# Optimization experiments

Hardware: AMD Instinct MI355X
Metric: run time of the kernel (lower is better)

The kernel has to match this reference:

```python
import jax, jax.numpy as jnp
import numpy as np

N = 100000      # num nodes
E = 800000      # num edges
IN = 256        # in_features
D = 64          # out_features per head
H = 4           # num_heads
EF = 64         # edge_feats
NET = 8         # num_etype
SLOPE = 0.2     # leaky relu negative slope


def setup_inputs() -> dict:
    key = jax.random.key(0)
    ks = jax.random.split(key, 12)
    s = 0.05
    h = jax.random.normal(ks[0], (N, IN), jnp.float32)
    row = jax.random.randint(ks[1], (E,), 0, N, dtype=jnp.int32)   # src
    col = jax.random.randint(ks[2], (E,), 0, N, dtype=jnp.int32)   # dst
    tp = jax.random.randint(ks[3], (E,), 0, NET, dtype=jnp.int32)  # edge type
    W = jax.random.normal(ks[4], (IN, D * H), jnp.float32) * s
    W_e = jax.random.normal(ks[5], (EF, EF * H), jnp.float32) * s
    edge_emb = jax.random.normal(ks[6], (NET, EF), jnp.float32) * s
    a_l = jax.random.normal(ks[7], (1, H, D), jnp.float32) * s
    a_r = jax.random.normal(ks[8], (1, H, D), jnp.float32) * s
    a_e = jax.random.normal(ks[9], (1, H, EF), jnp.float32) * s
    res_W = jax.random.normal(ks[10], (IN, D * H), jnp.float32) * s
    res_b = jnp.zeros((D * H,), jnp.float32)
    return {"h": h, "W": W, "W_e": W_e, "edge_emb": edge_emb,
            "a_l": a_l, "a_r": a_r, "a_e": a_e,
            "res_W": res_W, "res_b": res_b,
            "row": row, "col": col, "tp": tp}


def reference(h, W, W_e, edge_emb, a_l, a_r, a_e, res_W, res_b, row, col, tp):
    # node projection -> [N, H, D]; nan-guard as in the original
    emb = jnp.nan_to_num((h @ W).reshape(-1, H, D), nan=0.0)
    # edge-type embedding projection -> [NET, H, EF]
    e = (edge_emb @ W_e).reshape(-1, H, EF)
    # per-edge attention logits [E, H]
    h_l = (a_l * emb).sum(-1)[row]
    h_r = (a_r * emb).sum(-1)[col]
    h_e = (a_e * e).sum(-1)[tp]
    att = jax.nn.leaky_relu(h_l + h_r + h_e, SLOPE)
    # segment softmax over edges grouped by destination node
    m = jax.ops.segment_max(att, col, num_segments=N)          # [N, H]
    ex = jnp.exp(att - m[col])                                 # [E, H]
    denom = jax.ops.segment_sum(ex, col, num_segments=N)      # [N, H]
    alpha = ex / denom[col]                                    # [E, H]
    # gather-multiply-scatter message passing: [E, H, D] -> [N, H, D]
    msg = emb[row] * alpha[:, :, None]
    out = jax.ops.segment_sum(msg, col, num_segments=N).reshape(N, H * D)
    # residual linear + elu activation
    out = out + h @ res_W + res_b
    return jax.nn.elu(out)
```

## Files before the change

kernel.cpp:

```cpp
#include <hip/hip_runtime.h>

#define N_NODES 100000
#define E_EDGES 800000
#define IN_F 256
#define D_HEAD 64
#define H_HEADS 4
#define EF_F 64
#define NET_T 8
#define HD 256
#define SLOPE 0.2f
#define NTILES ((N_NODES + 63) / 64)

typedef unsigned short u16;
typedef unsigned long long u64;
typedef __attribute__((ext_vector_type(8))) short bf16x8;
typedef __attribute__((ext_vector_type(4))) float f32x4;

static __device__ __forceinline__ u16 f2bf(float f) {
    unsigned int u = __float_as_uint(f);
    unsigned int r = u + 0x7FFFu + ((u >> 16) & 1u);
    return (u16)(r >> 16);
}
static __device__ __forceinline__ float bf2f(unsigned int u) {
    return __uint_as_float(u << 16);
}

__global__ void k_se(const float* __restrict__ edge_emb, const float* __restrict__ W_e,
                     const float* __restrict__ a_e, float* __restrict__ s_e) {
    int tid = threadIdx.x;
    int t  = tid >> 5;
    int h  = (tid >> 3) & 3;
    int fc = tid & 7;
    float part = 0.f;
    for (int j = 0; j < 8; ++j) {
        int f = fc * 8 + j;
        float acc = 0.f;
        for (int k = 0; k < EF_F; ++k)
            acc += edge_emb[t * EF_F + k] * W_e[k * (EF_F * H_HEADS) + h * EF_F + f];
        part += a_e[h * EF_F + f] * acc;
    }
    for (int off = 1; off < 8; off <<= 1)
        part += __shfl_xor(part, off, 64);
    if (fc == 0) s_e[t * H_HEADS + h] = part;
}

__global__ void k_prep_w(const float* __restrict__ W, const float* __restrict__ resW,
                         u16* __restrict__ Bfrag) {
    const int gid = blockIdx.x * 256 + threadIdx.x;
    const int lane = gid & 63;
    const int fragid = gid >> 6;
    const int n = fragid & 3;
    const int ks = (fragid >> 2) & 7;
    const int g = fragid >> 5;
    const int c = g * 64 + n * 16 + (lane & 15);
    const int k0 = ks * 32 + (lane >> 4) * 8;
    const float* src = (c < HD) ? &W[c] : &resW[c - HD];
    u16 tmp[8];
#pragma unroll
    for (int j = 0; j < 8; ++j)
        tmp[j] = f2bf(src[(size_t)(k0 + j) * HD]);
    *reinterpret_cast<uint4*>(&Bfrag[(size_t)fragid * 512 + lane * 8]) =
        *reinterpret_cast<const uint4*>(tmp);
}

__global__ __launch_bounds__(256, 4)
void k_mfma(const float* __restrict__ A, const u16* __restrict__ Bfrag,
            const float* __restrict__ a_l, const float* __restrict__ a_r,
            const float* __restrict__ resb,
            u16* __restrict__ emb_bf, float* __restrict__ s_l, float* __restrict__ s_r,
            u16* __restrict__ res_bf) {
    __shared__ char At[32768];
    const int tid = threadIdx.x;
    const int lane = tid & 63;
    const int wv = tid >> 6;
    const int by = blockIdx.y;
    const int wid = (by << 2) | wv;
    const int row0 = blockIdx.x * 64;

#pragma unroll
    for (int c = 0; c < 16; ++c) {
        const int lin8 = c * 2048 + tid * 8;
        const int r_lin = lin8 >> 9;
        int grow = row0 + r_lin;
        if (grow >= N_NODES) grow = N_NODES - 1;
        const int colb = lin8 & 511;
        const float4 v = *reinterpret_cast<const float4*>(&A[(size_t)grow * IN_F + (colb >> 1)]);
        uint2 o;
        o.x = (unsigned)f2bf(v.x) | ((unsigned)f2bf(v.y) << 16);
        o.y = (unsigned)f2bf(v.z) | ((unsigned)f2bf(v.w) << 16);
        *reinterpret_cast<uint2*>(&At[lin8 ^ ((r_lin & 7) << 4)]) = o;
    }
    __syncthreads();

    const int lr = lane & 15;
    const int lg = lane >> 4;
    const int xr = (lr & 7) << 4;
    const int klg = lg * 16;

    int rowbase[4];
#pragma unroll
    for (int m = 0; m < 4; ++m) rowbase[m] = (m * 16 + lr) * 512;

    const u16* bp = Bfrag + (size_t)wid * 16384 + lane * 8;

    f32x4 acc[4][4] = {};
#pragma unroll
    for (int ks = 0; ks < 8; ++ks) {
        bf16x8 af[4], bfr[4];
        const int kx = ((ks << 6) + klg) ^ xr;
#pragma unroll
        for (int n = 0; n < 4; ++n)
            bfr[n] = *reinterpret_cast<const bf16x8*>(&bp[ks * 2048 + n * 512]);
#pragma unroll
        for (int m = 0; m < 4; ++m)
            af[m] = *reinterpret_cast<const bf16x8*>(&At[rowbase[m] + kx]);
#pragma unroll
        for (int m = 0; m < 4; ++m)
#pragma unroll
            for (int n = 0; n < 4; ++n)
                acc[m][n] = __builtin_amdgcn_mfma_f32_16x16x32_bf16(bfr[n], af[m], acc[m][n], 0, 0, 0);
    }

    if (by == 0) {
        const int h = wv;
        float4 alv[4], arv[4];
#pragma unroll
        for (int n = 0; n < 4; ++n) {
            alv[n] = *reinterpret_cast<const float4*>(&a_l[h * D_HEAD + n * 16 + lg * 4]);
            arv[n] = *reinterpret_cast<const float4*>(&a_r[h * D_HEAD + n * 16 + lg * 4]);
        }
#pragma unroll
        for (int m = 0; m < 4; ++m) {
            const int node = row0 + m * 16 + lr;
            float dl = 0.f, dr = 0.f;
            u64 pk[4];
#pragma unroll
            for (int n = 0; n < 4; ++n) {
                float v0 = acc[m][n][0], v1 = acc[m][n][1], v2 = acc[m][n][2], v3 = acc[m][n][3];
                v0 = isnan(v0) ? 0.f : v0;
                v1 = isnan(v1) ? 0.f : v1;
                v2 = isnan(v2) ? 0.f : v2;
                v3 = isnan(v3) ? 0.f : v3;
                dl += v0 * alv[n].x + v1 * alv[n].y + v2 * alv[n].z + v3 * alv[n].w;
                dr += v0 * arv[n].x + v1 * arv[n].y + v2 * arv[n].z + v3 * arv[n].w;
                pk[n] = (u64)f2bf(v0) | ((u64)f2bf(v1) << 16) |
                        ((u64)f2bf(v2) << 32) | ((u64)f2bf(v3) << 48);
            }
            if (node < N_NODES) {
                const size_t base = (size_t)node * HD + h * D_HEAD + lg * 4;
#pragma unroll
                for (int n = 0; n < 4; ++n)
                    *reinterpret_cast<u64*>(&emb_bf[base + n * 16]) = pk[n];
            }
            dl += __shfl_xor(dl, 16, 64); dr += __shfl_xor(dr, 16, 64);
            dl += __shfl_xor(dl, 32, 64); dr += __shfl_xor(dr, 32, 64);
            if (lg == 0 && node < N_NODES) {
                s_l[node * H_HEADS + h] = dl;
                s_r[node * H_HEADS + h] = dr;
            }
        }
    } else {
        const int c0 = wv * 64 + lg * 4;
        float4 rb[4];
#pragma unroll
        for (int n = 0; n < 4; ++n)
            rb[n] = *reinterpret_cast<const float4*>(&resb[c0 + n * 16]);
#pragma unroll
        for (int m = 0; m < 4; ++m) {
            const int node = row0 + m * 16 + lr;
            if (node < N_NODES) {
                const size_t base = (size_t)node * HD + c0;
#pragma unroll
                for (int n = 0; n < 4; ++n) {
                    const float v0 = acc[m][n][0] + rb[n].x;
                    const float v1 = acc[m][n][1] + rb[n].y;
                    const float v2 = acc[m][n][2] + rb[n].z;
                    const float v3 = acc[m][n][3] + rb[n].w;
                    const u64 pk = (u64)f2bf(v0) | ((u64)f2bf(v1) << 16) |
                                   ((u64)f2bf(v2) << 32) | ((u64)f2bf(v3) << 48);
                    *reinterpret_cast<u64*>(&res_bf[base + n * 16]) = pk;
                }
            }
        }
    }
}

__global__ void k_hist(const int* __restrict__ col, int* __restrict__ counts) {
    int e = blockIdx.x * 256 + threadIdx.x;
    if (e < E_EDGES) atomicAdd(&counts[col[e]], 1);
}

__global__ void k_scan1(const int* __restrict__ counts, int* __restrict__ row_ptr,
                        int* __restrict__ partials) {
    __shared__ int sd[256];
    const int t = threadIdx.x, b = blockIdx.x;
    const int base = b * 1024 + t * 4;
    int v[4];
#pragma unroll
    for (int j = 0; j < 4; ++j) v[j] = (base + j < N_NODES) ? counts[base + j] : 0;
    const int s = v[0] + v[1] + v[2] + v[3];
    sd[t] = s;
    __syncthreads();
    for (int off = 1; off < 256; off <<= 1) {
        int y = (t >= off) ? sd[t - off] : 0;
        __syncthreads();
        sd[t] += y;
        __syncthreads();
    }
    int p = sd[t] - s;
#pragma unroll
    for (int j = 0; j < 4; ++j) {
        if (base + j < N_NODES) row_ptr[base + j] = p;
        p += v[j];
    }
    if (t == 255) partials[b] = sd[255];
}

__global__ void k_scan2(int* __restrict__ partials) {
    __shared__ int sd[128];
    const int t = threadIdx.x;
    const int v = (t < 98) ? partials[t] : 0;
    sd[t] = v;
    __syncthreads();
    for (int off = 1; off < 128; off <<= 1) {
        int y = (t >= off) ? sd[t - off] : 0;
        __syncthreads();
        sd[t] += y;
        __syncthreads();
    }
    if (t < 98) partials[t] = sd[t] - v;
}

__global__ void k_scan3(int* __restrict__ row_ptr, int* __restrict__ fill,
                        const int* __restrict__ partials) {
    const int i = blockIdx.x * 256 + threadIdx.x;
    if (i < N_NODES) {
        const int v = row_ptr[i] + partials[i >> 10];
        row_ptr[i] = v;
        fill[i] = v;
    }
    if (i == 0) row_ptr[N_NODES] = E_EDGES;
}

__global__ void k_scatter(const int* __restrict__ row, const int* __restrict__ col,
                          const int* __restrict__ tp, const float* __restrict__ s_l,
                          const float* __restrict__ s_r, const float* __restrict__ s_e,
                          int* __restrict__ fill, int* __restrict__ perm_row,
                          float4* __restrict__ exw_perm) {
    const int e = blockIdx.x * 256 + threadIdx.x;
    if (e >= E_EDGES) return;
    const int r = row[e], c = col[e], t = tp[e];
    const float4 sl = *reinterpret_cast<const float4*>(&s_l[r * 4]);
    const float4 sr = *reinterpret_cast<const float4*>(&s_r[c * 4]);
    const float4 se = *reinterpret_cast<const float4*>(&s_e[t * 4]);
    float4 ex;
    float x;
    x = sl.x + sr.x + se.x; x = (x > 0.f) ? x : SLOPE * x; ex.x = __expf(x);
    x = sl.y + sr.y + se.y; x = (x > 0.f) ? x : SLOPE * x; ex.y = __expf(x);
    x = sl.z + sr.z + se.z; x = (x > 0.f) ? x : SLOPE * x; ex.z = __expf(x);
    x = sl.w + sr.w + se.w; x = (x > 0.f) ? x : SLOPE * x; ex.w = __expf(x);
    const int p = atomicAdd(&fill[c], 1);
    perm_row[p] = r;
    exw_perm[p] = ex;
}

__global__ __launch_bounds__(256)
void k_aggregate(const int* __restrict__ row_ptr, const int* __restrict__ perm_row,
                 const float* __restrict__ exw_perm,
                 const u16* __restrict__ emb_bf, const u16* __restrict__ res_bf,
                 float* __restrict__ outp) {
    const int wave = threadIdx.x >> 6;
    const int lane = threadIdx.x & 63;
    const int n = blockIdx.x * 4 + wave;
    const int h = lane >> 4;
    const int start = row_ptr[n], end = row_ptr[n + 1];
    const size_t o = (size_t)n * HD + lane * 4;
    const u64 rv = *reinterpret_cast<const u64*>(&res_bf[o]);

    float a0 = 0.f, a1 = 0.f, a2 = 0.f, a3 = 0.f, den = 0.f;
    int i = start;
    for (; i + 4 <= end; i += 4) {
        const int r0 = perm_row[i],     r1 = perm_row[i + 1];
        const int r2 = perm_row[i + 2], r3 = perm_row[i + 3];
        const float ex0 = exw_perm[(i)     * 4 + h];
        const float ex1 = exw_perm[(i + 1) * 4 + h];
        const float ex2 = exw_perm[(i + 2) * 4 + h];
        const float ex3 = exw_perm[(i + 3) * 4 + h];
        const u64 ev0 = *reinterpret_cast<const u64*>(&emb_bf[(size_t)r0 * HD + lane * 4]);
        const u64 ev1 = *reinterpret_cast<const u64*>(&emb_bf[(size_t)r1 * HD + lane * 4]);
        const u64 ev2 = *reinterpret_cast<const u64*>(&emb_bf[(size_t)r2 * HD + lane * 4]);
        const u64 ev3 = *reinterpret_cast<const u64*>(&emb_bf[(size_t)r3 * HD + lane * 4]);
        a0 += ex0 * bf2f((unsigned)(ev0) & 0xFFFFu)       + ex1 * bf2f((unsigned)(ev1) & 0xFFFFu)
            + ex2 * bf2f((unsigned)(ev2) & 0xFFFFu)       + ex3 * bf2f((unsigned)(ev3) & 0xFFFFu);
        a1 += ex0 * bf2f((unsigned)(ev0 >> 16) & 0xFFFFu) + ex1 * bf2f((unsigned)(ev1 >> 16) & 0xFFFFu)
            + ex2 * bf2f((unsigned)(ev2 >> 16) & 0xFFFFu) + ex3 * bf2f((unsigned)(ev3 >> 16) & 0xFFFFu);
        a2 += ex0 * bf2f((unsigned)(ev0 >> 32) & 0xFFFFu) + ex1 * bf2f((unsigned)(ev1 >> 32) & 0xFFFFu)
            + ex2 * bf2f((unsigned)(ev2 >> 32) & 0xFFFFu) + ex3 * bf2f((unsigned)(ev3 >> 32) & 0xFFFFu);
        a3 += ex0 * bf2f((unsigned)(ev0 >> 48) & 0xFFFFu) + ex1 * bf2f((unsigned)(ev1 >> 48) & 0xFFFFu)
            + ex2 * bf2f((unsigned)(ev2 >> 48) & 0xFFFFu) + ex3 * bf2f((unsigned)(ev3 >> 48) & 0xFFFFu);
        den += ex0 + ex1 + ex2 + ex3;
    }
    for (; i < end; ++i) {
        const int r0 = perm_row[i];
        const float ex0 = exw_perm[i * 4 + h];
        const u64 ev0 = *reinterpret_cast<const u64*>(&emb_bf[(size_t)r0 * HD + lane * 4]);
        a0 += ex0 * bf2f((unsigned)(ev0) & 0xFFFFu);
        a1 += ex0 * bf2f((unsigned)(ev0 >> 16) & 0xFFFFu);
        a2 += ex0 * bf2f((unsigned)(ev0 >> 32) & 0xFFFFu);
        a3 += ex0 * bf2f((unsigned)(ev0 >> 48) & 0xFFFFu);
        den += ex0;
    }
    const float inv = (den > 0.f) ? 1.f / den : 0.f;
    float4 out;
    float x;
    x = a0 * inv + bf2f((unsigned)(rv) & 0xFFFFu);       out.x = (x > 0.f) ? x : __expf(x) - 1.f;
    x = a1 * inv + bf2f((unsigned)(rv >> 16) & 0xFFFFu); out.y = (x > 0.f) ? x : __expf(x) - 1.f;
    x = a2 * inv + bf2f((unsigned)(rv >> 32) & 0xFFFFu); out.z = (x > 0.f) ? x : __expf(x) - 1.f;
    x = a3 * inv + bf2f((unsigned)(rv >> 48) & 0xFFFFu); out.w = (x > 0.f) ? x : __expf(x) - 1.f;
    *reinterpret_cast<float4*>(&outp[o]) = out;
}

extern "C" void kernel_launch(void* const* d_in, const int* in_sizes, int n_in,
                              void* d_out, int out_size, void* d_ws, size_t ws_size,
                              hipStream_t stream) {
    const float* h    = (const float*)d_in[0];
    const float* W    = (const float*)d_in[1];
    const float* W_e  = (const float*)d_in[2];
    const float* eemb = (const float*)d_in[3];
    const float* a_l  = (const float*)d_in[4];
    const float* a_r  = (const float*)d_in[5];
    const float* a_e  = (const float*)d_in[6];
    const float* resW = (const float*)d_in[7];
    const float* resb = (const float*)d_in[8];
    const int* row = (const int*)d_in[9];
    const int* col = (const int*)d_in[10];
    const int* tp  = (const int*)d_in[11];
    float* outp = (float*)d_out;

    char* ws = (char*)d_ws;
    size_t off = 0;
    auto alloc = [&](size_t b) { size_t o = off; off += (b + 255) & ~(size_t)255; return o; };
    u16*  Bfrag   = (u16*)(ws + alloc((size_t)512 * IN_F * 2));
    u16*  emb_bf  = (u16*)(ws + alloc((size_t)N_NODES * HD * 2));
    u16*  res_bf  = (u16*)(ws + alloc((size_t)N_NODES * HD * 2));
    float* s_l    = (float*)(ws + alloc((size_t)N_NODES * H_HEADS * 4));
    float* s_r    = (float*)(ws + alloc((size_t)N_NODES * H_HEADS * 4));
    float* s_e    = (float*)(ws + alloc(NET_T * H_HEADS * 4));
    int*  counts  = (int*)(ws + alloc((size_t)N_NODES * 4));
    int*  row_ptr = (int*)(ws + alloc((size_t)(N_NODES + 1) * 4));
    int*  fill    = (int*)(ws + alloc((size_t)N_NODES * 4));
    int*  perm_row= (int*)(ws + alloc((size_t)E_EDGES * 4));
    float* exw_perm=(float*)(ws + alloc((size_t)E_EDGES * H_HEADS * 4));
    int*  partials= (int*)(ws + alloc(128 * 4));

    k_se<<<1, 256, 0, stream>>>(eemb, W_e, a_e, s_e);
    k_prep_w<<<64, 256, 0, stream>>>(W, resW, Bfrag);
    dim3 g2(NTILES, 2);
    k_mfma<<<g2, 256, 0, stream>>>(h, Bfrag, a_l, a_r, resb, emb_bf, s_l, s_r, res_bf);
    hipMemsetAsync(counts, 0, (size_t)N_NODES * 4, stream);
    k_hist<<<(E_EDGES + 255) / 256, 256, 0, stream>>>(col, counts);
    k_scan1<<<98, 256, 0, stream>>>(counts, row_ptr, partials);
    k_scan2<<<1, 128, 0, stream>>>(partials);
    k_scan3<<<(N_NODES + 255) / 256, 256, 0, stream>>>(row_ptr, fill, partials);
    k_scatter<<<(E_EDGES + 255) / 256, 256, 0, stream>>>(row, col, tp, s_l, s_r, s_e,
                                                         fill, perm_row, (float4*)exw_perm);
    k_aggregate<<<N_NODES / 4, 256, 0, stream>>>(row_ptr, perm_row, exw_perm, emb_bf, res_bf, outp);
}
```

Before: 308.7 us.

## Interleave MFMA grid halves, simplify bf16 unpack, nontemporal output stores

The GEMM grid becomes 1D, with the two column halves of each row tile placed in adjacent blocks. This should let both halves share the same h rows in L2 around the same time. The aggregate kernel now unpacks bf16 pairs with a single shift or mask per value instead of shift, mask and shift. The final output is written with nontemporal stores so it does not pollute cache. The changes are small, and the nontemporal stores might affect caching for later readers.

Result: faster. 296.6 us (-3.9%).

```diff
diff --git a/kernel.cpp b/kernel.cpp
--- a/kernel.cpp
+++ b/kernel.cpp
@@ -73,9 +73,9 @@
     const int tid = threadIdx.x;
     const int lane = tid & 63;
     const int wv = tid >> 6;
-    const int by = blockIdx.y;
+    const int by = blockIdx.x & 1;
     const int wid = (by << 2) | wv;
-    const int row0 = blockIdx.x * 64;
+    const int row0 = (blockIdx.x >> 1) * 64;
 
 #pragma unroll
     for (int c = 0; c < 16; ++c) {
@@ -290,34 +290,39 @@
         const u64 ev1 = *reinterpret_cast<const u64*>(&emb_bf[(size_t)r1 * HD + lane * 4]);
         const u64 ev2 = *reinterpret_cast<const u64*>(&emb_bf[(size_t)r2 * HD + lane * 4]);
         const u64 ev3 = *reinterpret_cast<const u64*>(&emb_bf[(size_t)r3 * HD + lane * 4]);
-        a0 += ex0 * bf2f((unsigned)(ev0) & 0xFFFFu)       + ex1 * bf2f((unsigned)(ev1) & 0xFFFFu)
-            + ex2 * bf2f((unsigned)(ev2) & 0xFFFFu)       + ex3 * bf2f((unsigned)(ev3) & 0xFFFFu);
-        a1 += ex0 * bf2f((unsigned)(ev0 >> 16) & 0xFFFFu) + ex1 * bf2f((unsigned)(ev1 >> 16) & 0xFFFFu)
-            + ex2 * bf2f((unsigned)(ev2 >> 16) & 0xFFFFu) + ex3 * bf2f((unsigned)(ev3 >> 16) & 0xFFFFu);
-        a2 += ex0 * bf2f((unsigned)(ev0 >> 32) & 0xFFFFu) + ex1 * bf2f((unsigned)(ev1 >> 32) & 0xFFFFu)
-            + ex2 * bf2f((unsigned)(ev2 >> 32) & 0xFFFFu) + ex3 * bf2f((unsigned)(ev3 >> 32) & 0xFFFFu);
-        a3 += ex0 * bf2f((unsigned)(ev0 >> 48) & 0xFFFFu) + ex1 * bf2f((unsigned)(ev1 >> 48) & 0xFFFFu)
-            + ex2 * bf2f((unsigned)(ev2 >> 48) & 0xFFFFu) + ex3 * bf2f((unsigned)(ev3 >> 48) & 0xFFFFu);
+        const unsigned l0 = (unsigned)ev0, h0 = (unsigned)(ev0 >> 32);
+        const unsigned l1 = (unsigned)ev1, h1 = (unsigned)(ev1 >> 32);
+        const unsigned l2 = (unsigned)ev2, h2 = (unsigned)(ev2 >> 32);
+        const unsigned l3 = (unsigned)ev3, h3 = (unsigned)(ev3 >> 32);
+        a0 += ex0 * __uint_as_float(l0 << 16)          + ex1 * __uint_as_float(l1 << 16)
+            + ex2 * __uint_as_float(l2 << 16)          + ex3 * __uint_as_float(l3 << 16);
+        a1 += ex0 * __uint_as_float(l0 & 0xFFFF0000u)  + ex1 * __uint_as_float(l1 & 0xFFFF0000u)
+            + ex2 * __uint_as_float(l2 & 0xFFFF0000u)  + ex3 * __uint_as_float(l3 & 0xFFFF0000u);
+        a2 += ex0 * __uint_as_float(h0 << 16)          + ex1 * __uint_as_float(h1 << 16)
+            + ex2 * __uint_as_float(h2 << 16)          + ex3 * __uint_as_float(h3 << 16);
+        a3 += ex0 * __uint_as_float(h0 & 0xFFFF0000u)  + ex1 * __uint_as_float(h1 & 0xFFFF0000u)
+            + ex2 * __uint_as_float(h2 & 0xFFFF0000u)  + ex3 * __uint_as_float(h3 & 0xFFFF0000u);
         den += ex0 + ex1 + ex2 + ex3;
     }
     for (; i < end; ++i) {
         const int r0 = perm_row[i];
         const float ex0 = exw_perm[i * 4 + h];
         const u64 ev0 = *reinterpret_cast<const u64*>(&emb_bf[(size_t)r0 * HD + lane * 4]);
-        a0 += ex0 * bf2f((unsigned)(ev0) & 0xFFFFu);
-        a1 += ex0 * bf2f((unsigned)(ev0 >> 16) & 0xFFFFu);
-        a2 += ex0 * bf2f((unsigned)(ev0 >> 32) & 0xFFFFu);
-        a3 += ex0 * bf2f((unsigned)(ev0 >> 48) & 0xFFFFu);
+        const unsigned l0 = (unsigned)ev0, h0 = (unsigned)(ev0 >> 32);
+        a0 += ex0 * __uint_as_float(l0 << 16);
+        a1 += ex0 * __uint_as_float(l0 & 0xFFFF0000u);
+        a2 += ex0 * __uint_as_float(h0 << 16);
+        a3 += ex0 * __uint_as_float(h0 & 0xFFFF0000u);
         den += ex0;
     }
     const float inv = (den > 0.f) ? 1.f / den : 0.f;
-    float4 out;
+    f32x4 out;
     float x;
     x = a0 * inv + bf2f((unsigned)(rv) & 0xFFFFu);       out.x = (x > 0.f) ? x : __expf(x) - 1.f;
     x = a1 * inv + bf2f((unsigned)(rv >> 16) & 0xFFFFu); out.y = (x > 0.f) ? x : __expf(x) - 1.f;
     x = a2 * inv + bf2f((unsigned)(rv >> 32) & 0xFFFFu); out.z = (x > 0.f) ? x : __expf(x) - 1.f;
     x = a3 * inv + bf2f((unsigned)(rv >> 48) & 0xFFFFu); out.w = (x > 0.f) ? x : __expf(x) - 1.f;
-    *reinterpret_cast<float4*>(&outp[o]) = out;
+    __builtin_nontemporal_store(out, reinterpret_cast<f32x4*>(&outp[o]));
 }
 
 extern "C" void kernel_launch(void* const* d_in, const int* in_sizes, int n_in,
@@ -355,9 +360,8 @@
 
     k_se<<<1, 256, 0, stream>>>(eemb, W_e, a_e, s_e);
     k_prep_w<<<64, 256, 0, stream>>>(W, resW, Bfrag);
-    dim3 g2(NTILES, 2);
-    k_mfma<<<g2, 256, 0, stream>>>(h, Bfrag, a_l, a_r, resb, emb_bf, s_l, s_r, res_bf);
-    hipMemsetAsync(counts, 0, (size_t)N_NODES * 4, stream);
+    k_mfma<<<NTILES * 2, 256, 0, stream>>>(h, Bfrag, a_l, a_r, resb, emb_bf, s_l, s_r, res_bf);
+    (void)hipMemsetAsync(counts, 0, (size_t)N_NODES * 4, stream);
     k_hist<<<(E_EDGES + 255) / 256, 256, 0, stream>>>(col, counts);
     k_scan1<<<98, 256, 0, stream>>>(counts, row_ptr, partials);
     k_scan2<<<1, 128, 0, stream>>>(partials);
```
